# Optimization experiments

Measured on AMD Instinct MI355X. Metric: run time of the kernel, lower is better.

## Reference

```python
import jax, jax.numpy as jnp
import numpy as np

HIDDEN = 1024
NUM_HEADS = 16
HEAD_DIM = HIDDEN // NUM_HEADS  # 64
ROPE_DIM = HEAD_DIM // 2        # 32 (per-axis rotary dim)
EPS = 1e-6


def _make_rope_tables(dim, grid_h, grid_w, theta=10000.0):
    # pt_seq_len == ft_seq_len, so t_h = arange(H), t_w = arange(W)
    freqs = 1.0 / theta ** (np.arange(0, dim, 2, dtype=np.float32)[: dim // 2] / dim)  # [dim//2]
    fh = np.repeat(np.outer(np.arange(grid_h, dtype=np.float32), freqs), 2, axis=-1)  # [H, dim]
    fw = np.repeat(np.outer(np.arange(grid_w, dtype=np.float32), freqs), 2, axis=-1)  # [W, dim]
    fh = np.broadcast_to(fh[:, None, :], (grid_h, grid_w, dim))
    fw = np.broadcast_to(fw[None, :, :], (grid_h, grid_w, dim))
    f2d = np.concatenate([fh, fw], axis=-1).reshape(grid_h * grid_w, 2 * dim)  # [HW, 2*dim]
    return jnp.asarray(np.cos(f2d)), jnp.asarray(np.sin(f2d))


def _rms_norm(x, w, eps=EPS):
    var = jnp.mean(jnp.square(x), axis=-1, keepdims=True)
    return x * jax.lax.rsqrt(var + eps) * w


def _rotate_half(x):
    x1 = x[..., 0::2]
    x2 = x[..., 1::2]
    return jnp.stack([-x2, x1], axis=-1).reshape(x.shape)


def _apply_rope(x, cos, sin):
    # x: [B, H, S, D]; cos/sin: [S, D]
    return x * cos + _rotate_half(x) * sin


def setup_inputs() -> dict:
    key = jax.random.key(0)
    ks = jax.random.split(key, 12)
    B, IMG_H, IMG_W, CND_H, CND_W = 2, 64, 64, 32, 32
    img_len, cnd_len = IMG_H * IMG_W, CND_H * CND_W
    xav = (6.0 / (HIDDEN + HIDDEN)) ** 0.5
    inp = {
        'image_tokens': jax.random.normal(ks[0], (B, img_len, HIDDEN), jnp.float32),
        'condition_tokens': jax.random.normal(ks[1], (B, cnd_len, HIDDEN), jnp.float32),
        'q_norm_w': jnp.ones((HIDDEN,), jnp.float32),
        'kv_norm_w': jnp.ones((HIDDEN,), jnp.float32),
        'q_head_norm_w': jnp.ones((HEAD_DIM,), jnp.float32),
        'k_head_norm_w': jnp.ones((HEAD_DIM,), jnp.float32),
        'q_w': jax.random.uniform(ks[2], (HIDDEN, HIDDEN), jnp.float32, -xav, xav),
        'q_b': jnp.zeros((HIDDEN,), jnp.float32),
        'k_w': jax.random.uniform(ks[3], (HIDDEN, HIDDEN), jnp.float32, -xav, xav),
        'k_b': jnp.zeros((HIDDEN,), jnp.float32),
        'v_w': jax.random.uniform(ks[4], (HIDDEN, HIDDEN), jnp.float32, -xav, xav),
        'v_b': jnp.zeros((HIDDEN,), jnp.float32),
        'o_w': jax.random.uniform(ks[5], (HIDDEN, HIDDEN), jnp.float32, -xav, xav),
        'o_b': jnp.zeros((HIDDEN,), jnp.float32),
        'alpha': jnp.full((1,), 0.5, jnp.float32),  # nonzero so backward exercises the attn path
    }
    ic, isn = _make_rope_tables(ROPE_DIM, IMG_H, IMG_W)
    cc, cs = _make_rope_tables(ROPE_DIM, CND_H, CND_W)
    inp.update(image_cos=ic, image_sin=isn, cond_cos=cc, cond_sin=cs)
    return inp


def reference(image_tokens, condition_tokens, q_norm_w, kv_norm_w, q_head_norm_w,
              k_head_norm_w, q_w, q_b, k_w, k_b, v_w, v_b, o_w, o_b, alpha,
              image_cos, image_sin, cond_cos, cond_sin):
    B, Li, _ = image_tokens.shape
    Lc = condition_tokens.shape[1]
    qn = _rms_norm(image_tokens, q_norm_w)
    kvn = _rms_norm(condition_tokens, kv_norm_w)
    # projections (torch Linear: x @ W.T + b); weights here stored [out, in]
    q = (qn @ q_w.T + q_b).reshape(B, Li, NUM_HEADS, HEAD_DIM).transpose(0, 2, 1, 3)
    k = (kvn @ k_w.T + k_b).reshape(B, Lc, NUM_HEADS, HEAD_DIM).transpose(0, 2, 1, 3)
    v = (kvn @ v_w.T + v_b).reshape(B, Lc, NUM_HEADS, HEAD_DIM).transpose(0, 2, 1, 3)
    q = _rms_norm(q, q_head_norm_w)
    k = _rms_norm(k, k_head_norm_w)
    q = _apply_rope(q, image_cos, image_sin)
    k = _apply_rope(k, cond_cos, cond_sin)
    scale = 1.0 / jnp.sqrt(jnp.asarray(HEAD_DIM, q.dtype))
    scores = jnp.einsum('bhqd,bhkd->bhqk', q, k) * scale
    attn = jax.nn.softmax(scores, axis=-1)
    out = jnp.einsum('bhqk,bhkd->bhqd', attn, v)
    out = out.transpose(0, 2, 1, 3).reshape(B, Li, HIDDEN)
    update = out @ o_w.T + o_b
    return image_tokens + alpha.reshape(1, 1, 1) * update
```

## Files before the change

kernel.cpp:

```cpp
#include <hip/hip_runtime.h>

typedef __bf16 bf16x8 __attribute__((ext_vector_type(8)));
typedef __bf16 bf16x4 __attribute__((ext_vector_type(4)));
typedef float  f32x4  __attribute__((ext_vector_type(4)));
typedef float  f32x16 __attribute__((ext_vector_type(16)));
typedef unsigned u32x2 __attribute__((ext_vector_type(2)));

#define DEVINL __device__ __forceinline__

DEVINL void gload_lds16(const void* g, void* l) {
  __builtin_amdgcn_global_load_lds((const __attribute__((address_space(1))) void*)g,
                                   (__attribute__((address_space(3))) void*)l, 16, 0, 0);
}

DEVINL unsigned pkbf(float a, float b) {
  union { __bf16 h[2]; unsigned u; } c;
  c.h[0] = (__bf16)a; c.h[1] = (__bf16)b;
  return c.u;
}

DEVINL float fast_exp2(float x) {
#if __has_builtin(__builtin_amdgcn_exp2f)
  return __builtin_amdgcn_exp2f(x);
#else
  float r;
  asm volatile("v_exp_f32 %0, %1" : "=v"(r) : "v"(x));
  return r;
#endif
}

DEVINL float2 swap32(float x) {
  u32x2 r = __builtin_amdgcn_permlane32_swap(__float_as_uint(x), __float_as_uint(x), false, false);
  return make_float2(__uint_as_float(r.x), __uint_as_float(r.y));
}

__global__ __launch_bounds__(256) void prep_kernel(
    const float* __restrict__ XA, const float* __restrict__ WA, __bf16* __restrict__ YA,
    const float* __restrict__ XB, const float* __restrict__ WB, __bf16* __restrict__ YB,
    const float* __restrict__ wq, const float* __restrict__ wk,
    const float* __restrict__ wv, const float* __restrict__ wo,
    __bf16* __restrict__ oq, __bf16* __restrict__ ok,
    __bf16* __restrict__ ov, __bf16* __restrict__ oo) {
  int rb = blockIdx.x, tid = threadIdx.x;
  if (rb < 10240) {
    const float* X; const float* W; __bf16* Y; int row;
    if (rb < 8192) { X = XA; W = WA; Y = YA; row = rb; }
    else { X = XB; W = WB; Y = YB; row = rb - 8192; }
    const float4* xr = (const float4*)(X + (size_t)row * 1024);
    float4 v = xr[tid];
    float ss = v.x * v.x + v.y * v.y + v.z * v.z + v.w * v.w;
#pragma unroll
    for (int m = 1; m < 64; m <<= 1) ss += __shfl_xor(ss, m);
    __shared__ float part[4];
    if ((tid & 63) == 0) part[tid >> 6] = ss;
    __syncthreads();
    float tot = part[0] + part[1] + part[2] + part[3];
    float rn = rsqrtf(tot * (1.0f / 1024.0f) + 1e-6f);
    float4 wv4 = ((const float4*)W)[tid];
    bf16x4 y;
    y[0] = (__bf16)(v.x * rn * wv4.x);
    y[1] = (__bf16)(v.y * rn * wv4.y);
    y[2] = (__bf16)(v.z * rn * wv4.z);
    y[3] = (__bf16)(v.w * rn * wv4.w);
    *(bf16x4*)(Y + (size_t)row * 1024 + tid * 4) = y;
  } else {
    int gid = (rb - 10240) * 256 + tid;
    int which = gid >> 17;
    size_t off = (size_t)(gid & 131071) * 8;
    const float* s = (which == 0) ? wq : (which == 1) ? wk : (which == 2) ? wv : wo;
    __bf16* o = (which == 0) ? oq : (which == 1) ? ok : (which == 2) ? ov : oo;
    float4 v0 = *(const float4*)(s + off), v1 = *(const float4*)(s + off + 4);
    bf16x8 y;
    y[0] = (__bf16)v0.x; y[1] = (__bf16)v0.y; y[2] = (__bf16)v0.z; y[3] = (__bf16)v0.w;
    y[4] = (__bf16)v1.x; y[5] = (__bf16)v1.y; y[6] = (__bf16)v1.z; y[7] = (__bf16)v1.w;
    *(bf16x8*)(o + off) = y;
  }
}

template <typename EPIF>
DEVINL void gemm_core(const __bf16* __restrict__ A, const __bf16* __restrict__ Bw,
                      int m0, int n0, char* AsB, char* BsB, EPIF epi) {
  int tid = threadIdx.x, lane = tid & 63, w = tid >> 6, wr = w >> 1, wc = w & 1;
  f32x4 z4 = {0.f, 0.f, 0.f, 0.f};
  f32x4 acc[4][4];
#pragma unroll
  for (int i = 0; i < 4; i++)
#pragma unroll
    for (int j = 0; j < 4; j++) acc[i][j] = z4;

  auto STAGE = [&](int k0, int bsel) {
#pragma unroll
    for (int i = 0; i < 2; i++) {
      int chunk = i * 256 + tid;
      int row = chunk >> 2, cc = chunk & 3;
      gload_lds16(A + (size_t)(m0 + row) * 1024 + k0 + cc * 8,
                  AsB + bsel * 8192 + i * 4096 + w * 1024);
      gload_lds16(Bw + (size_t)(n0 + row) * 1024 + k0 + cc * 8,
                  BsB + bsel * 8192 + i * 4096 + w * 1024);
    }
  };

  STAGE(0, 0);
  int b = 0;
  for (int it = 0; it < 32; ++it) {
    if (it < 31) {
      STAGE((it + 1) * 32, b ^ 1);
      asm volatile("s_waitcnt vmcnt(4)" ::: "memory");
    } else {
      asm volatile("s_waitcnt vmcnt(0)" ::: "memory");
    }
    __builtin_amdgcn_s_barrier();
    asm volatile("" ::: "memory");
    const char* As = AsB + b * 8192;
    const char* Bs = BsB + b * 8192;
    bf16x8 af[4], bfr[4];
#pragma unroll
    for (int m = 0; m < 4; m++) {
      int r = wr * 64 + m * 16 + (lane & 15);
      af[m] = *(const bf16x8*)(As + r * 64 + ((lane >> 4) << 4));
    }
#pragma unroll
    for (int n = 0; n < 4; n++) {
      int r = wc * 64 + n * 16 + (lane & 15);
      bfr[n] = *(const bf16x8*)(Bs + r * 64 + ((lane >> 4) << 4));
    }
    __builtin_amdgcn_s_setprio(1);
#pragma unroll
    for (int m = 0; m < 4; m++)
#pragma unroll
      for (int n = 0; n < 4; n++)
        acc[m][n] = __builtin_amdgcn_mfma_f32_16x16x32_bf16(af[m], bfr[n], acc[m][n], 0, 0, 0);
    __builtin_amdgcn_s_setprio(0);
    __builtin_amdgcn_s_barrier();
    asm volatile("" ::: "memory");
    b ^= 1;
  }
  epi(acc, lane, wr, wc);
}

__global__ __launch_bounds__(256) void qkv_gemm_kernel(
    const __bf16* __restrict__ qn, const __bf16* __restrict__ kvn,
    const __bf16* __restrict__ wq, const __bf16* __restrict__ wkv,
    const float* __restrict__ qb, const float* __restrict__ kb, const float* __restrict__ vb,
    __bf16* __restrict__ Qt, __bf16* __restrict__ Kt, __bf16* __restrict__ Vt0) {
  __shared__ __attribute__((aligned(16))) char AsB[2 * 8192];
  __shared__ __attribute__((aligned(16))) char BsB[2 * 8192];
  int id = blockIdx.x;
  const __bf16 *A, *Bw; const float* bias; __bf16* Cout;
  int m0, n0, nloc;
  if (id < 512) {
    A = qn; Bw = wq; m0 = (id & 63) * 128; n0 = (id >> 6) * 128; nloc = n0;
    bias = qb; Cout = Qt;
  } else {
    int i2 = id - 512;
    A = kvn; Bw = wkv; m0 = (i2 & 15) * 128; n0 = (i2 >> 4) * 128;
    if (n0 < 1024) { bias = kb; Cout = Kt; nloc = n0; }
    else { bias = vb; Cout = Vt0; nloc = n0 - 1024; }
  }
  gemm_core(A, Bw, m0, n0, AsB, BsB,
            [&](f32x4 (&acc)[4][4], int lane, int wr, int wc) {
#pragma unroll
              for (int m = 0; m < 4; m++)
#pragma unroll
                for (int n = 0; n < 4; n++) {
                  int col = nloc + wc * 64 + n * 16 + (lane & 15);
                  float bv = bias[col];
#pragma unroll
                  for (int r = 0; r < 4; r++) {
                    int row = m0 + wr * 64 + m * 16 + ((lane >> 4) << 2) + r;
                    Cout[((size_t)row << 10) + col] = (__bf16)(acc[m][n][r] + bv);
                  }
                }
            });
}

__global__ __launch_bounds__(256) void gemm_o_kernel(
    const __bf16* __restrict__ A, const __bf16* __restrict__ Bw,
    const float* __restrict__ bias, float* __restrict__ Cout,
    const float* __restrict__ resid, const float* __restrict__ alphap) {
  __shared__ __attribute__((aligned(16))) char AsB[2 * 8192];
  __shared__ __attribute__((aligned(16))) char BsB[2 * 8192];
  int m0 = blockIdx.x * 128, n0 = blockIdx.y * 128;
  float aval = alphap[0];
  gemm_core(A, Bw, m0, n0, AsB, BsB,
            [&](f32x4 (&acc)[4][4], int lane, int wr, int wc) {
#pragma unroll
              for (int m = 0; m < 4; m++)
#pragma unroll
                for (int n = 0; n < 4; n++) {
                  int col = n0 + wc * 64 + n * 16 + (lane & 15);
                  float bv = bias[col];
#pragma unroll
                  for (int r = 0; r < 4; r++) {
                    int row = m0 + wr * 64 + m * 16 + ((lane >> 4) << 2) + r;
                    size_t idx = ((size_t)row << 10) + col;
                    Cout[idx] = resid[idx] + aval * (acc[m][n][r] + bv);
                  }
                }
            });
}

__global__ __launch_bounds__(256) void kprep_kernel(
    const __bf16* __restrict__ Kt, const float* __restrict__ KHW,
    const float* __restrict__ CCOS, const float* __restrict__ CSIN,
    __bf16* __restrict__ Kr,
    const __bf16* __restrict__ V, __bf16* __restrict__ Vt) {
  int rb = blockIdx.x, tid = threadIdx.x;
  if (rb < 1024) {
    int inst = rb * 32 + (tid >> 3);
    int sub = tid & 7;
    int token = inst >> 4, h = inst & 15;
    int b = token >> 10, pos = token & 1023;
    const __bf16* xp = Kt + ((size_t)token << 10) + h * 64 + sub * 8;
    bf16x8 xv = *(const bf16x8*)xp;
    float xf[8];
#pragma unroll
    for (int i = 0; i < 8; i++) xf[i] = (float)xv[i];
    float ss = 0.f;
#pragma unroll
    for (int i = 0; i < 8; i++) ss += xf[i] * xf[i];
    ss += __shfl_xor(ss, 1);
    ss += __shfl_xor(ss, 2);
    ss += __shfl_xor(ss, 4);
    float rn = rsqrtf(ss * (1.0f / 64.0f) + 1e-6f);
    const float* hwp = KHW + sub * 8;
    const float* cp = CCOS + ((size_t)pos << 6) + sub * 8;
    const float* sp = CSIN + ((size_t)pos << 6) + sub * 8;
    float xn[8], o[8];
#pragma unroll
    for (int i = 0; i < 8; i++) xn[i] = xf[i] * rn * hwp[i];
#pragma unroll
    for (int i = 0; i < 8; i += 2) {
      o[i] = xn[i] * cp[i] - xn[i + 1] * sp[i];
      o[i + 1] = xn[i + 1] * cp[i + 1] + xn[i] * sp[i + 1];
    }
    bf16x8 yv;
#pragma unroll
    for (int i = 0; i < 8; i++) yv[i] = (__bf16)o[i];
    *(bf16x8*)(Kr + (((size_t)((b << 4) + h) << 10) + pos) * 64 + sub * 8) = yv;
  } else {
    int bx = rb - 1024;
    int bh = bx >> 4;
    int j0 = (bx & 15) * 64;
    int b = bh >> 4, h = bh & 15;
#pragma unroll
    for (int it = 0; it < 2; ++it) {
      int c = it * 256 + tid;
      int jl = c >> 3, d0 = (c & 7) * 8;
      bf16x8 v = *(const bf16x8*)(V + (size_t)(b * 1024 + j0 + jl) * 1024 + h * 64 + d0);
#pragma unroll
      for (int i = 0; i < 8; i++)
        Vt[((size_t)bh * 64 + d0 + i) * 1024 + j0 + jl] = v[i];
    }
  }
}

__global__ __launch_bounds__(256, 4) void attn_kernel(
    const __bf16* __restrict__ Qt, const float* __restrict__ QHW,
    const float* __restrict__ QCOS, const float* __restrict__ QSIN,
    const __bf16* __restrict__ Kr, const __bf16* __restrict__ Vtr,
    __bf16* __restrict__ AO) {
  int tid = threadIdx.x, lane = tid & 63, w = tid >> 6;
  int lq = lane & 31, hi = lane >> 5;
  int wgid = blockIdx.x;
  int nid = (wgid & 7) * 128 + (wgid >> 3);
  int q0 = (nid & 31) * 128;
  int bh = nid >> 5, b = bh >> 4, h = bh & 15;
  const float QSC = 0.125f * 1.44269504088896340736f;

  __shared__ __attribute__((aligned(16))) __bf16 Ks[2][4096];
  __shared__ __attribute__((aligned(16))) __bf16 Vs[2][4096];

  int s0 = 2 * w, s1 = 2 * w + 1;
  const __bf16* kSrc0 = Kr + ((size_t)bh << 16) + (size_t)((s0 >> 2) * 32 + lq) * 64 + (s0 & 3) * 16 + hi * 8;
  const __bf16* kSrc1 = Kr + ((size_t)bh << 16) + (size_t)((s1 >> 2) * 32 + lq) * 64 + (s1 & 3) * 16 + hi * 8;
  const __bf16* vSrc0 = Vtr + ((size_t)bh << 16) + (size_t)((s0 & 1) * 32 + lq) * 1024 + (s0 >> 1) * 16 + hi * 8;
  const __bf16* vSrc1 = Vtr + ((size_t)bh << 16) + (size_t)((s1 & 1) * 32 + lq) * 1024 + (s1 >> 1) * 16 + hi * 8;

  auto STAGE = [&](int T, int BSEL) {
    gload_lds16(kSrc0 + (size_t)T * 4096, (char*)Ks[BSEL] + s0 * 1024);
    gload_lds16(kSrc1 + (size_t)T * 4096, (char*)Ks[BSEL] + s1 * 1024);
    gload_lds16(vSrc0 + T * 64, (char*)Vs[BSEL] + s0 * 1024);
    gload_lds16(vSrc1 + T * 64, (char*)Vs[BSEL] + s1 * 1024);
  };

  STAGE(0, 0);

  bf16x8 qf[4];
  {
    int pos = q0 + w * 32 + lq;
    const __bf16* qp = Qt + ((size_t)(b * 4096 + pos) << 10) + h * 64 + hi * 8;
    float xf[4][8];
    float ss = 0.f;
#pragma unroll
    for (int ds = 0; ds < 4; ds++) {
      bf16x8 xv = *(const bf16x8*)(qp + ds * 16);
#pragma unroll
      for (int j = 0; j < 8; j++) { float f = (float)xv[j]; xf[ds][j] = f; ss += f * f; }
    }
    float2 sw = swap32(ss);
    float rn = rsqrtf((sw.x + sw.y) * (1.0f / 64.0f) + 1e-6f);
#pragma unroll
    for (int ds = 0; ds < 4; ds++) {
      int d0 = ds * 16 + hi * 8;
      const float* wp = QHW + d0;
      const float* cp = QCOS + ((size_t)pos << 6) + d0;
      const float* sp = QSIN + ((size_t)pos << 6) + d0;
      float4 wa = *(const float4*)wp, wb = *(const float4*)(wp + 4);
      float4 ca = *(const float4*)cp, cb = *(const float4*)(cp + 4);
      float4 sa = *(const float4*)sp, sb = *(const float4*)(sp + 4);
      float wv[8] = {wa.x, wa.y, wa.z, wa.w, wb.x, wb.y, wb.z, wb.w};
      float cv[8] = {ca.x, ca.y, ca.z, ca.w, cb.x, cb.y, cb.z, cb.w};
      float sv[8] = {sa.x, sa.y, sa.z, sa.w, sb.x, sb.y, sb.z, sb.w};
      float xn[8];
#pragma unroll
      for (int j = 0; j < 8; j++) xn[j] = xf[ds][j] * rn * wv[j];
      bf16x8 q8;
#pragma unroll
      for (int j = 0; j < 8; j += 2) {
        q8[j]     = (__bf16)((xn[j] * cv[j] - xn[j + 1] * sv[j]) * QSC);
        q8[j + 1] = (__bf16)((xn[j + 1] * cv[j + 1] + xn[j] * sv[j + 1]) * QSC);
      }
      qf[ds] = q8;
    }
  }

  f32x16 Z16;
#pragma unroll
  for (int r = 0; r < 16; r++) Z16[r] = 0.f;
  f32x16 accO[2];
  accO[0] = Z16; accO[1] = Z16;
  float srun = 0.f;
  int loff = lane * 16;

  int buf = 0;
  for (int t = 0; t < 16; t++) {
    if (t < 15) {
      STAGE(t + 1, buf ^ 1);
      asm volatile("s_waitcnt vmcnt(4)" ::: "memory");
    } else {
      asm volatile("s_waitcnt vmcnt(0)" ::: "memory");
    }
    __builtin_amdgcn_s_barrier();
    asm volatile("" ::: "memory");

    const char* kbase = (const char*)Ks[buf];
    const char* vbase = (const char*)Vs[buf];

    unsigned pa[4][4];
    float ssum = 0.f;

    bf16x8 kfA[4];
#pragma unroll
    for (int s = 0; s < 4; s++) kfA[s] = *(const bf16x8*)(kbase + s * 1024 + loff);
    f32x16 accS;
    __builtin_amdgcn_s_setprio(1);
    accS = __builtin_amdgcn_mfma_f32_32x32x16_bf16(kfA[0], qf[0], Z16, 0, 0, 0);
#pragma unroll
    for (int ds = 1; ds < 4; ds++)
      accS = __builtin_amdgcn_mfma_f32_32x32x16_bf16(kfA[ds], qf[ds], accS, 0, 0, 0);
    __builtin_amdgcn_s_setprio(0);

    bf16x8 kfB[4];
#pragma unroll
    for (int s = 0; s < 4; s++) kfB[s] = *(const bf16x8*)(kbase + (4 + s) * 1024 + loff);

#pragma unroll
    for (int r = 0; r < 16; r++) {
      float e = fast_exp2(accS[r]);
      accS[r] = e;
      ssum += e;
    }
#pragma unroll
    for (int s2 = 0; s2 < 2; s2++) {
      int rb = s2 * 8;
      unsigned u  = pkbf(accS[rb + 0], accS[rb + 1]);
      unsigned v2 = pkbf(accS[rb + 2], accS[rb + 3]);
      unsigned w2 = pkbf(accS[rb + 4], accS[rb + 5]);
      unsigned x2 = pkbf(accS[rb + 6], accS[rb + 7]);
      u32x2 r02 = __builtin_amdgcn_permlane32_swap(u, w2, false, false);
      u32x2 r13 = __builtin_amdgcn_permlane32_swap(v2, x2, false, false);
      pa[s2][0] = r02.x; pa[s2][1] = r13.x; pa[s2][2] = r02.y; pa[s2][3] = r13.y;
    }

    __builtin_amdgcn_s_setprio(1);
    accS = __builtin_amdgcn_mfma_f32_32x32x16_bf16(kfB[0], qf[0], Z16, 0, 0, 0);
#pragma unroll
    for (int ds = 1; ds < 4; ds++)
      accS = __builtin_amdgcn_mfma_f32_32x32x16_bf16(kfB[ds], qf[ds], accS, 0, 0, 0);
    __builtin_amdgcn_s_setprio(0);

    bf16x8 vf[8];
#pragma unroll
    for (int s = 0; s < 8; s++) vf[s] = *(const bf16x8*)(vbase + s * 1024 + loff);

#pragma unroll
    for (int r = 0; r < 16; r++) {
      float e = fast_exp2(accS[r]);
      accS[r] = e;
      ssum += e;
    }
#pragma unroll
    for (int s2 = 0; s2 < 2; s2++) {
      int rb = s2 * 8;
      unsigned u  = pkbf(accS[rb + 0], accS[rb + 1]);
      unsigned v2 = pkbf(accS[rb + 2], accS[rb + 3]);
      unsigned w2 = pkbf(accS[rb + 4], accS[rb + 5]);
      unsigned x2 = pkbf(accS[rb + 6], accS[rb + 7]);
      u32x2 r02 = __builtin_amdgcn_permlane32_swap(u, w2, false, false);
      u32x2 r13 = __builtin_amdgcn_permlane32_swap(v2, x2, false, false);
      pa[2 + s2][0] = r02.x; pa[2 + s2][1] = r13.x; pa[2 + s2][2] = r02.y; pa[2 + s2][3] = r13.y;
    }

    float2 sws = swap32(ssum);
    srun += sws.x + sws.y;

    __builtin_amdgcn_s_setprio(1);
#pragma unroll
    for (int f = 0; f < 4; f++) {
      union { unsigned u[4]; bf16x8 v; } pf;
      pf.u[0] = pa[f][0]; pf.u[1] = pa[f][1]; pf.u[2] = pa[f][2]; pf.u[3] = pa[f][3];
#pragma unroll
      for (int dh = 0; dh < 2; dh++)
        accO[dh] = __builtin_amdgcn_mfma_f32_32x32x16_bf16(pf.v, vf[f * 2 + dh], accO[dh], 0, 0, 0);
    }
    __builtin_amdgcn_s_setprio(0);

    __builtin_amdgcn_s_barrier();
    asm volatile("" ::: "memory");
    buf ^= 1;
  }

  __bf16* aobase = AO + (((size_t)b * 4096) << 10) + h * 64;
  float rinv = 1.0f / srun;
  int ri = __float_as_int(rinv);
#pragma unroll
  for (int r = 0; r < 16; r++) {
    int cr = (r & 3) + ((r >> 2) << 3) + (hi << 2);
    float rv = __int_as_float(__builtin_amdgcn_ds_bpermute(cr << 2, ri));
    size_t rowoff = ((size_t)(q0 + w * 32 + cr) << 10);
#pragma unroll
    for (int dh = 0; dh < 2; dh++)
      aobase[rowoff + dh * 32 + lq] = (__bf16)(accO[dh][r] * rv);
  }
}

extern "C" void kernel_launch(void* const* d_in, const int* in_sizes, int n_in,
                              void* d_out, int out_size, void* d_ws, size_t ws_size,
                              hipStream_t stream) {
  const float* img  = (const float*)d_in[0];
  const float* cnd  = (const float*)d_in[1];
  const float* qnw  = (const float*)d_in[2];
  const float* kvnw = (const float*)d_in[3];
  const float* qhw  = (const float*)d_in[4];
  const float* khw  = (const float*)d_in[5];
  const float* qw   = (const float*)d_in[6];
  const float* qb   = (const float*)d_in[7];
  const float* kw   = (const float*)d_in[8];
  const float* kb   = (const float*)d_in[9];
  const float* vw   = (const float*)d_in[10];
  const float* vb   = (const float*)d_in[11];
  const float* ow   = (const float*)d_in[12];
  const float* ob   = (const float*)d_in[13];
  const float* alpha= (const float*)d_in[14];
  const float* icos = (const float*)d_in[15];
  const float* isin = (const float*)d_in[16];
  const float* ccos = (const float*)d_in[17];
  const float* csin = (const float*)d_in[18];
  float* out = (float*)d_out;

  __bf16* p = (__bf16*)d_ws;
  __bf16* wqb = p; p += 1048576;
  __bf16* wkb = p; p += 1048576;
  __bf16* wvb = p; p += 1048576;
  __bf16* wob = p; p += 1048576;
  __bf16* qn  = p; p += 8388608;
  __bf16* kvn = p; p += 2097152;
  __bf16* Qt  = p; p += 8388608;
  __bf16* Kt  = p; p += 2097152;
  __bf16* Vt0 = p; p += 2097152;
  __bf16* Kr  = p; p += 2097152;
  __bf16* Vtr = p; p += 2097152;
  __bf16* AO  = qn;

  prep_kernel<<<12288, 256, 0, stream>>>(img, qnw, qn, cnd, kvnw, kvn,
                                         qw, kw, vw, ow, wqb, wkb, wvb, wob);

  qkv_gemm_kernel<<<768, 256, 0, stream>>>(qn, kvn, wqb, wkb, qb, kb, vb, Qt, Kt, Vt0);

  kprep_kernel<<<1536, 256, 0, stream>>>(Kt, khw, ccos, csin, Kr, Vt0, Vtr);

  attn_kernel<<<1024, 256, 0, stream>>>(Qt, qhw, icos, isin, Kr, Vtr, AO);

  gemm_o_kernel<<<dim3(64, 8), 256, 0, stream>>>(AO, wob, ob, out, img, alpha);
}
```

Baseline: 152.3 us.

## Replace LDS-staged K/V with per-wave register prefetch in attention kernel

Attention workgroups shrink from four waves sharing K/V tiles in LDS to single-wave blocks that load K and V fragments directly from global memory into registers. The next tile is prefetched while computing the current one, with explicit vmcnt waits. This removes LDS staging and workgroup barriers but gives up K/V sharing across waves, quadrupling global/L2 read traffic for K/V and raising register pressure.

After: 216.2 us. +41.9%, slower.

```diff
diff --git a/kernel.cpp b/kernel.cpp
--- a/kernel.cpp
+++ b/kernel.cpp
@@ -12,6 +12,19 @@
   __builtin_amdgcn_global_load_lds((const __attribute__((address_space(1))) void*)g,
                                    (__attribute__((address_space(3))) void*)l, 16, 0, 0);
 }
+
+DEVINL bf16x8 gload16(unsigned voff, const __bf16* sbase) {
+  bf16x8 r;
+  asm volatile("global_load_dwordx4 %0, %1, %2"
+               : "=v"(r)
+               : "v"(voff), "s"(sbase)
+               : "memory");
+  return r;
+}
+
+#define VM_WAIT(n)                                           \
+  asm volatile("s_waitcnt vmcnt(" #n ")" ::: "memory");      \
+  __builtin_amdgcn_sched_barrier(0)
 
 DEVINL unsigned pkbf(float a, float b) {
   union { __bf16 h[2]; unsigned u; } c;
@@ -255,40 +268,32 @@
   }
 }
 
-__global__ __launch_bounds__(256, 4) void attn_kernel(
+__global__ __launch_bounds__(64) void attn_kernel(
     const __bf16* __restrict__ Qt, const float* __restrict__ QHW,
     const float* __restrict__ QCOS, const float* __restrict__ QSIN,
     const __bf16* __restrict__ Kr, const __bf16* __restrict__ Vtr,
     __bf16* __restrict__ AO) {
-  int tid = threadIdx.x, lane = tid & 63, w = tid >> 6;
+  int lane = threadIdx.x & 63;
   int lq = lane & 31, hi = lane >> 5;
   int wgid = blockIdx.x;
-  int nid = (wgid & 7) * 128 + (wgid >> 3);
-  int q0 = (nid & 31) * 128;
-  int bh = nid >> 5, b = bh >> 4, h = bh & 15;
+  int nid = (wgid & 7) * 512 + (wgid >> 3);
+  int bh = nid >> 7, q0 = (nid & 127) * 32;
+  int b = bh >> 4, h = bh & 15;
   const float QSC = 0.125f * 1.44269504088896340736f;
 
-  __shared__ __attribute__((aligned(16))) __bf16 Ks[2][4096];
-  __shared__ __attribute__((aligned(16))) __bf16 Vs[2][4096];
-
-  int s0 = 2 * w, s1 = 2 * w + 1;
-  const __bf16* kSrc0 = Kr + ((size_t)bh << 16) + (size_t)((s0 >> 2) * 32 + lq) * 64 + (s0 & 3) * 16 + hi * 8;
-  const __bf16* kSrc1 = Kr + ((size_t)bh << 16) + (size_t)((s1 >> 2) * 32 + lq) * 64 + (s1 & 3) * 16 + hi * 8;
-  const __bf16* vSrc0 = Vtr + ((size_t)bh << 16) + (size_t)((s0 & 1) * 32 + lq) * 1024 + (s0 >> 1) * 16 + hi * 8;
-  const __bf16* vSrc1 = Vtr + ((size_t)bh << 16) + (size_t)((s1 & 1) * 32 + lq) * 1024 + (s1 >> 1) * 16 + hi * 8;
-
-  auto STAGE = [&](int T, int BSEL) {
-    gload_lds16(kSrc0 + (size_t)T * 4096, (char*)Ks[BSEL] + s0 * 1024);
-    gload_lds16(kSrc1 + (size_t)T * 4096, (char*)Ks[BSEL] + s1 * 1024);
-    gload_lds16(vSrc0 + T * 64, (char*)Vs[BSEL] + s0 * 1024);
-    gload_lds16(vSrc1 + T * 64, (char*)Vs[BSEL] + s1 * 1024);
-  };
-
-  STAGE(0, 0);
+  const __bf16* Kb = Kr + ((size_t)bh << 16);
+  const __bf16* Vb = Vtr + ((size_t)bh << 16);
+
+  unsigned kvo[8], vvo[8];
+#pragma unroll
+  for (int s = 0; s < 8; s++) {
+    kvo[s] = (unsigned)((((s >> 2) * 32 + lq) * 64 + (s & 3) * 16 + hi * 8) * 2);
+    vvo[s] = (unsigned)((((s & 1) * 32 + lq) * 1024 + (s >> 1) * 16 + hi * 8) * 2);
+  }
 
   bf16x8 qf[4];
   {
-    int pos = q0 + w * 32 + lq;
+    int pos = q0 + lq;
     const __bf16* qp = Qt + ((size_t)(b * 4096 + pos) << 10) + h * 64 + hi * 8;
     float xf[4][8];
     float ss = 0.f;
@@ -331,39 +336,28 @@
   f32x16 accO[2];
   accO[0] = Z16; accO[1] = Z16;
   float srun = 0.f;
-  int loff = lane * 16;
-
-  int buf = 0;
+
+  asm volatile("s_waitcnt vmcnt(0)" ::: "memory");
+
+  bf16x8 kf[8], vf[8];
+#pragma unroll
+  for (int s = 0; s < 8; s++) kf[s] = gload16(kvo[s], Kb);
+#pragma unroll
+  for (int s = 0; s < 8; s++) vf[s] = gload16(vvo[s], Vb);
+
   for (int t = 0; t < 16; t++) {
-    if (t < 15) {
-      STAGE(t + 1, buf ^ 1);
-      asm volatile("s_waitcnt vmcnt(4)" ::: "memory");
-    } else {
-      asm volatile("s_waitcnt vmcnt(0)" ::: "memory");
-    }
-    __builtin_amdgcn_s_barrier();
-    asm volatile("" ::: "memory");
-
-    const char* kbase = (const char*)Ks[buf];
-    const char* vbase = (const char*)Vs[buf];
+    VM_WAIT(8);
 
     unsigned pa[4][4];
     float ssum = 0.f;
 
-    bf16x8 kfA[4];
-#pragma unroll
-    for (int s = 0; s < 4; s++) kfA[s] = *(const bf16x8*)(kbase + s * 1024 + loff);
     f32x16 accS;
     __builtin_amdgcn_s_setprio(1);
-    accS = __builtin_amdgcn_mfma_f32_32x32x16_bf16(kfA[0], qf[0], Z16, 0, 0, 0);
-#pragma unroll
-    for (int ds = 1; ds < 4; ds++)
-      accS = __builtin_amdgcn_mfma_f32_32x32x16_bf16(kfA[ds], qf[ds], accS, 0, 0, 0);
+    accS = __builtin_amdgcn_mfma_f32_32x32x16_bf16(kf[0], qf[0], Z16, 0, 0, 0);
+    accS = __builtin_amdgcn_mfma_f32_32x32x16_bf16(kf[1], qf[1], accS, 0, 0, 0);
+    accS = __builtin_amdgcn_mfma_f32_32x32x16_bf16(kf[2], qf[2], accS, 0, 0, 0);
+    accS = __builtin_amdgcn_mfma_f32_32x32x16_bf16(kf[3], qf[3], accS, 0, 0, 0);
     __builtin_amdgcn_s_setprio(0);
-
-    bf16x8 kfB[4];
-#pragma unroll
-    for (int s = 0; s < 4; s++) kfB[s] = *(const bf16x8*)(kbase + (4 + s) * 1024 + loff);
 
 #pragma unroll
     for (int r = 0; r < 16; r++) {
@@ -373,26 +367,28 @@
     }
 #pragma unroll
     for (int s2 = 0; s2 < 2; s2++) {
-      int rb = s2 * 8;
-      unsigned u  = pkbf(accS[rb + 0], accS[rb + 1]);
-      unsigned v2 = pkbf(accS[rb + 2], accS[rb + 3]);
-      unsigned w2 = pkbf(accS[rb + 4], accS[rb + 5]);
-      unsigned x2 = pkbf(accS[rb + 6], accS[rb + 7]);
+      int rb2 = s2 * 8;
+      unsigned u  = pkbf(accS[rb2 + 0], accS[rb2 + 1]);
+      unsigned v2 = pkbf(accS[rb2 + 2], accS[rb2 + 3]);
+      unsigned w2 = pkbf(accS[rb2 + 4], accS[rb2 + 5]);
+      unsigned x2 = pkbf(accS[rb2 + 6], accS[rb2 + 7]);
       u32x2 r02 = __builtin_amdgcn_permlane32_swap(u, w2, false, false);
       u32x2 r13 = __builtin_amdgcn_permlane32_swap(v2, x2, false, false);
       pa[s2][0] = r02.x; pa[s2][1] = r13.x; pa[s2][2] = r02.y; pa[s2][3] = r13.y;
     }
 
     __builtin_amdgcn_s_setprio(1);
-    accS = __builtin_amdgcn_mfma_f32_32x32x16_bf16(kfB[0], qf[0], Z16, 0, 0, 0);
-#pragma unroll
-    for (int ds = 1; ds < 4; ds++)
-      accS = __builtin_amdgcn_mfma_f32_32x32x16_bf16(kfB[ds], qf[ds], accS, 0, 0, 0);
+    accS = __builtin_amdgcn_mfma_f32_32x32x16_bf16(kf[4], qf[0], Z16, 0, 0, 0);
+    accS = __builtin_amdgcn_mfma_f32_32x32x16_bf16(kf[5], qf[1], accS, 0, 0, 0);
+    accS = __builtin_amdgcn_mfma_f32_32x32x16_bf16(kf[6], qf[2], accS, 0, 0, 0);
+    accS = __builtin_amdgcn_mfma_f32_32x32x16_bf16(kf[7], qf[3], accS, 0, 0, 0);
     __builtin_amdgcn_s_setprio(0);
 
-    bf16x8 vf[8];
-#pragma unroll
-    for (int s = 0; s < 8; s++) vf[s] = *(const bf16x8*)(vbase + s * 1024 + loff);
+    if (t < 15) {
+      const __bf16* kb2 = Kb + (size_t)(t + 1) * 4096;
+#pragma unroll
+      for (int s = 0; s < 8; s++) kf[s] = gload16(kvo[s], kb2);
+    }
 
 #pragma unroll
     for (int r = 0; r < 16; r++) {
@@ -402,11 +398,11 @@
     }
 #pragma unroll
     for (int s2 = 0; s2 < 2; s2++) {
-      int rb = s2 * 8;
-      unsigned u  = pkbf(accS[rb + 0], accS[rb + 1]);
-      unsigned v2 = pkbf(accS[rb + 2], accS[rb + 3]);
-      unsigned w2 = pkbf(accS[rb + 4], accS[rb + 5]);
-      unsigned x2 = pkbf(accS[rb + 6], accS[rb + 7]);
+      int rb2 = s2 * 8;
+      unsigned u  = pkbf(accS[rb2 + 0], accS[rb2 + 1]);
+      unsigned v2 = pkbf(accS[rb2 + 2], accS[rb2 + 3]);
+      unsigned w2 = pkbf(accS[rb2 + 4], accS[rb2 + 5]);
+      unsigned x2 = pkbf(accS[rb2 + 6], accS[rb2 + 7]);
       u32x2 r02 = __builtin_amdgcn_permlane32_swap(u, w2, false, false);
       u32x2 r13 = __builtin_amdgcn_permlane32_swap(v2, x2, false, false);
       pa[2 + s2][0] = r02.x; pa[2 + s2][1] = r13.x; pa[2 + s2][2] = r02.y; pa[2 + s2][3] = r13.y;
@@ -415,20 +411,35 @@
     float2 sws = swap32(ssum);
     srun += sws.x + sws.y;
 
+    if (t < 15) {
+      VM_WAIT(8);
+    } else {
+      VM_WAIT(0);
+    }
+
     __builtin_amdgcn_s_setprio(1);
-#pragma unroll
-    for (int f = 0; f < 4; f++) {
+    {
       union { unsigned u[4]; bf16x8 v; } pf;
-      pf.u[0] = pa[f][0]; pf.u[1] = pa[f][1]; pf.u[2] = pa[f][2]; pf.u[3] = pa[f][3];
-#pragma unroll
-      for (int dh = 0; dh < 2; dh++)
-        accO[dh] = __builtin_amdgcn_mfma_f32_32x32x16_bf16(pf.v, vf[f * 2 + dh], accO[dh], 0, 0, 0);
+      pf.u[0] = pa[0][0]; pf.u[1] = pa[0][1]; pf.u[2] = pa[0][2]; pf.u[3] = pa[0][3];
+      accO[0] = __builtin_amdgcn_mfma_f32_32x32x16_bf16(pf.v, vf[0], accO[0], 0, 0, 0);
+      accO[1] = __builtin_amdgcn_mfma_f32_32x32x16_bf16(pf.v, vf[1], accO[1], 0, 0, 0);
+      pf.u[0] = pa[1][0]; pf.u[1] = pa[1][1]; pf.u[2] = pa[1][2]; pf.u[3] = pa[1][3];
+      accO[0] = __builtin_amdgcn_mfma_f32_32x32x16_bf16(pf.v, vf[2], accO[0], 0, 0, 0);
+      accO[1] = __builtin_amdgcn_mfma_f32_32x32x16_bf16(pf.v, vf[3], accO[1], 0, 0, 0);
+      pf.u[0] = pa[2][0]; pf.u[1] = pa[2][1]; pf.u[2] = pa[2][2]; pf.u[3] = pa[2][3];
+      accO[0] = __builtin_amdgcn_mfma_f32_32x32x16_bf16(pf.v, vf[4], accO[0], 0, 0, 0);
+      accO[1] = __builtin_amdgcn_mfma_f32_32x32x16_bf16(pf.v, vf[5], accO[1], 0, 0, 0);
+      pf.u[0] = pa[3][0]; pf.u[1] = pa[3][1]; pf.u[2] = pa[3][2]; pf.u[3] = pa[3][3];
+      accO[0] = __builtin_amdgcn_mfma_f32_32x32x16_bf16(pf.v, vf[6], accO[0], 0, 0, 0);
+      accO[1] = __builtin_amdgcn_mfma_f32_32x32x16_bf16(pf.v, vf[7], accO[1], 0, 0, 0);
     }
     __builtin_amdgcn_s_setprio(0);
 
-    __builtin_amdgcn_s_barrier();
-    asm volatile("" ::: "memory");
-    buf ^= 1;
+    if (t < 15) {
+      const __bf16* vb2 = Vb + (t + 1) * 64;
+#pragma unroll
+      for (int s = 0; s < 8; s++) vf[s] = gload16(vvo[s], vb2);
+    }
   }
 
   __bf16* aobase = AO + (((size_t)b * 4096) << 10) + h * 64;
@@ -438,7 +449,7 @@
   for (int r = 0; r < 16; r++) {
     int cr = (r & 3) + ((r >> 2) << 3) + (hi << 2);
     float rv = __int_as_float(__builtin_amdgcn_ds_bpermute(cr << 2, ri));
-    size_t rowoff = ((size_t)(q0 + w * 32 + cr) << 10);
+    size_t rowoff = ((size_t)(q0 + cr) << 10);
 #pragma unroll
     for (int dh = 0; dh < 2; dh++)
       aobase[rowoff + dh * 32 + lq] = (__bf16)(accO[dh][r] * rv);
@@ -490,7 +501,7 @@
 
   kprep_kernel<<<1536, 256, 0, stream>>>(Kt, khw, ccos, csin, Kr, Vt0, Vtr);
 
-  attn_kernel<<<1024, 256, 0, stream>>>(Qt, qhw, icos, isin, Kr, Vtr, AO);
+  attn_kernel<<<4096, 64, 0, stream>>>(Qt, qhw, icos, isin, Kr, Vtr, AO);
 
   gemm_o_kernel<<<dim3(64, 8), 256, 0, stream>>>(AO, wob, ob, out, img, alpha);
 }
```
